# Optimization experiments

Hardware: AMD Instinct MI355X
Metric: run time of the kernel (lower is better)

Reference implementation:

```python
import math
import jax, jax.numpy as jnp
import numpy as np

LARGE_NEG_F32 = -9000000000000000.0  # matches torch code for float32 logits


def setup_inputs() -> dict:
    key = jax.random.key(0)
    ks = jax.random.split(key, 6)
    B, S, D, H = 4, 2048, 1024, 16
    scale = 1.0 / math.sqrt(D)
    query = jax.random.normal(ks[0], (B, S, D), dtype=jnp.float32)
    Wq = jax.random.normal(ks[1], (D, D), dtype=jnp.float32) * scale
    Wk = jax.random.normal(ks[2], (D, D), dtype=jnp.float32) * scale
    Wv = jax.random.normal(ks[3], (D, D), dtype=jnp.float32) * scale
    Wo = jax.random.normal(ks[4], (D, D), dtype=jnp.float32) * scale
    bq = jnp.zeros((D,), jnp.float32)
    bk = jnp.zeros((D,), jnp.float32)
    bv = jnp.zeros((D,), jnp.float32)
    bo = jnp.zeros((D,), jnp.float32)
    padding_mask = jnp.ones((B, S), dtype=jnp.int32)
    causal_mask = jnp.tril(jnp.ones((S, S), dtype=jnp.int32))[None, None]  # [1,1,S,S]
    return {
        "query": query, "padding_mask": padding_mask, "causal_mask": causal_mask,
        "Wq": Wq, "bq": bq, "Wk": Wk, "bk": bk, "Wv": Wv, "bv": bv, "Wo": Wo, "bo": bo,
    }


def reference(query, padding_mask, causal_mask, Wq, bq, Wk, bk, Wv, bv, Wo, bo):
    B, S, D = query.shape
    H = 16
    dh = D // H
    # torch Linear: y = x @ W.T + b  (W stored as [out, in])
    q = query @ Wq.T + bq
    k = query @ Wk.T + bk   # value defaults to query (self-attention)
    v = query @ Wv.T + bv
    # [B, H, S, dh]
    q = q.reshape(B, S, H, dh).transpose(0, 2, 1, 3)
    k = k.reshape(B, S, H, dh).transpose(0, 2, 1, 3)
    v = v.reshape(B, S, H, dh).transpose(0, 2, 1, 3)
    logits = jnp.einsum("bhqd,bhkd->bhqk", q, k) / math.sqrt(dh)
    pad = padding_mask[:, None, None, :]            # [B,1,1,S]
    logits = jnp.where(pad == 0, LARGE_NEG_F32, logits)
    logits = jnp.where(causal_mask == 0, LARGE_NEG_F32, logits)
    weights = jax.nn.softmax(logits, axis=-1)
    out = jnp.einsum("bhqk,bhkd->bhqd", weights, v)
    out = out.transpose(0, 2, 1, 3).reshape(B, S, D)
    out = out @ Wo.T + bo
    return out, weights
```

## Files before the change

kernel.cpp:

```cpp
#include <hip/hip_runtime.h>
#include <stdint.h>


typedef unsigned short u16;
typedef __attribute__((ext_vector_type(8))) short s16x8;
typedef __attribute__((ext_vector_type(4))) float f32x4;

#define BQ 4
#define SQ 2048
#define DQ 1024
#define HQ 16
#define DH 64
#define BSD (BQ * SQ * DQ)

__device__ __forceinline__ u16 f2bf(float f) {
  union { float f; uint32_t u; } x; x.f = f;
  uint32_t r = (x.u + 0x7fffu + ((x.u >> 16) & 1u)) >> 16;
  return (u16)r;
}

template <typename TA>
__global__ __launch_bounds__(256, 2)
void gemm_bt(const TA* __restrict__ A,
             const float* __restrict__ W0, const float* __restrict__ W1, const float* __restrict__ W2,
             const float* __restrict__ b0, const float* __restrict__ b1, const float* __restrict__ b2,
             void* __restrict__ o0, void* __restrict__ o1, void* __restrict__ o2,
             int qkv) {
  const int z = blockIdx.z;
  const float* W    = (z == 0) ? W0 : (z == 1) ? W1 : W2;
  const float* bias = (z == 0) ? b0 : (z == 1) ? b1 : b2;
  void* out         = (z == 0) ? o0 : (z == 1) ? o1 : o2;
  const int mode = qkv ? ((z == 2) ? 1 : 0) : 2;

  const int n0 = blockIdx.x * 128;
  const int m0 = blockIdx.y * 128;
  const int tid = threadIdx.x;
  const int wv = tid >> 6, lane = tid & 63;
  const int wm = wv >> 1, wn = wv & 1;
  const int lr = lane & 15, lg = lane >> 4;

  __shared__ alignas(16) u16 Alds[128 * 64];
  __shared__ alignas(16) u16 Blds[128 * 64];

  const TA* Ablk = A + (size_t)m0 * 1024;
  const float* Wblk = W + (size_t)n0 * 1024;

  f32x4 acc[4][4] = {};

  for (int k0 = 0; k0 < 1024; k0 += 64) {
    __syncthreads();
#pragma unroll
    for (int p = 0; p < 4; ++p) {
      int s = p * 256 + tid;
      int r = s >> 3, c = s & 7;
      int cs = c ^ (r & 7);
      if constexpr (sizeof(TA) == 4) {
        const float* src = (const float*)&Ablk[(size_t)r * 1024 + k0 + c * 8];
        f32x4 a0 = *(const f32x4*)&src[0];
        f32x4 a1 = *(const f32x4*)&src[4];
        s16x8 hv;
#pragma unroll
        for (int j = 0; j < 4; ++j) { hv[j] = (short)f2bf(a0[j]); hv[4 + j] = (short)f2bf(a1[j]); }
        *(s16x8*)&Alds[r * 64 + cs * 8] = hv;
      } else {
        *(s16x8*)&Alds[r * 64 + cs * 8] = *(const s16x8*)&Ablk[(size_t)r * 1024 + k0 + c * 8];
      }
      {
        const float* src = &Wblk[(size_t)r * 1024 + k0 + c * 8];
        f32x4 a0 = *(const f32x4*)&src[0];
        f32x4 a1 = *(const f32x4*)&src[4];
        s16x8 hv;
#pragma unroll
        for (int j = 0; j < 4; ++j) { hv[j] = (short)f2bf(a0[j]); hv[4 + j] = (short)f2bf(a1[j]); }
        *(s16x8*)&Blds[r * 64 + cs * 8] = hv;
      }
    }
    __syncthreads();

#pragma unroll
    for (int half = 0; half < 2; ++half) {
      s16x8 af[4], bf[4];
#pragma unroll
      for (int mt = 0; mt < 4; ++mt) {
        int r = wm * 64 + mt * 16 + lr;
        int cc = (half * 4 + lg) ^ (r & 7);
        af[mt] = *(const s16x8*)&Alds[r * 64 + cc * 8];
      }
#pragma unroll
      for (int nt = 0; nt < 4; ++nt) {
        int r = wn * 64 + nt * 16 + lr;
        int cc = (half * 4 + lg) ^ (r & 7);
        bf[nt] = *(const s16x8*)&Blds[r * 64 + cc * 8];
      }
#pragma unroll
      for (int mt = 0; mt < 4; ++mt)
#pragma unroll
        for (int nt = 0; nt < 4; ++nt)
          acc[mt][nt] = __builtin_amdgcn_mfma_f32_16x16x32_bf16(af[mt], bf[nt], acc[mt][nt], 0, 0, 0);
    }
  }

#pragma unroll
  for (int nt = 0; nt < 4; ++nt) {
    int n = n0 + wn * 64 + nt * 16 + lr;
    float bv = bias[n];
#pragma unroll
    for (int mt = 0; mt < 4; ++mt) {
#pragma unroll
      for (int j = 0; j < 4; ++j) {
        int m = m0 + wm * 64 + mt * 16 + lg * 4 + j;
        float v = acc[mt][nt][j] + bv;
        int s = m & 2047, h = n >> 6, c = n & 63;
        if (mode == 0) {
          int bb = m >> 11;
          ((u16*)out)[(((size_t)bb * HQ + h) * SQ + s) * DH + c] = f2bf(v);
        } else if (mode == 1) {
          int bb = m >> 11;
          ((u16*)out)[(((size_t)bb * HQ + h) * DH + c) * SQ + s] = f2bf(v);
        } else {
          ((float*)out)[(size_t)m * DQ + n] = v;
        }
      }
    }
  }
}

__global__ __launch_bounds__(256, 4)
void attn_kernel(const u16* __restrict__ Qh, const u16* __restrict__ Kh,
                 const u16* __restrict__ Vt, const int* __restrict__ pad,
                 float* __restrict__ Wout, u16* __restrict__ ctx) {
  const int bh = blockIdx.y;
  const int qt = (int)((blockIdx.x + bh) & 31);
  const int b = bh >> 4, h = bh & 15;
  const int tid = threadIdx.x, wv = tid >> 6, lane = tid & 63;
  const int lr = lane & 15, lg = lane >> 4;

  __shared__ alignas(16) float Plds[4][16][68];

  const u16* Qb = Qh + (size_t)bh * SQ * DH;
  const u16* Kb = Kh + (size_t)bh * SQ * DH;
  const u16* Vb = Vt + (size_t)bh * DH * SQ;
  const int* pb = pad + b * SQ;

  const float SCL = 0.125f;
  const float SENT = -30000.0f;

  const int q0 = qt * 64 + wv * 16;

  const s16x8 qf0 = *(const s16x8*)&Qb[(q0 + lr) * DH + lg * 8];
  const s16x8 qf1 = *(const s16x8*)&Qb[(q0 + lr) * DH + 32 + lg * 8];

  auto loadK = [&](int kt, s16x8* a, s16x8* b2) {
    const u16* Kt = Kb + kt * 64 * DH;
#pragma unroll
    for (int kc = 0; kc < 4; ++kc) {
      a[kc]  = *(const s16x8*)&Kt[(kc * 16 + lr) * DH + lg * 8];
      b2[kc] = *(const s16x8*)&Kt[(kc * 16 + lr) * DH + 32 + lg * 8];
    }
  };

  float l[4] = {0.f, 0.f, 0.f, 0.f};
  {
    s16x8 kA[4], kB[4], kC[4], kD[4];
    auto body1 = [&](const s16x8* a, const s16x8* b2, int kt) {
#pragma unroll
      for (int kc = 0; kc < 4; ++kc) {
        f32x4 zz = {0.f, 0.f, 0.f, 0.f};
        f32x4 s = __builtin_amdgcn_mfma_f32_16x16x32_bf16(qf0, a[kc], zz, 0, 0, 0);
        s = __builtin_amdgcn_mfma_f32_16x16x32_bf16(qf1, b2[kc], s, 0, 0, 0);
        int kcol = kt * 64 + kc * 16 + lr;
        bool padz = (pb[kcol] == 0);
#pragma unroll
        for (int j = 0; j < 4; ++j) {
          int qrow = q0 + lg * 4 + j;
          float t = (padz || kcol > qrow) ? SENT : s[j] * SCL;
          l[j] += __expf(t);
        }
      }
    };
    loadK(0, kA, kB);
    for (int kt = 0; kt <= qt; kt += 2) {
      if (kt + 1 <= qt) loadK(kt + 1, kC, kD);
      body1(kA, kB, kt);
      if (kt + 1 <= qt) {
        if (kt + 2 <= qt) loadK(kt + 2, kA, kB);
        body1(kC, kD, kt + 1);
      }
    }
  }

  float invL[4];
#pragma unroll
  for (int j = 0; j < 4; ++j) {
    float la = l[j];
    la += __shfl_xor(la, 1);
    la += __shfl_xor(la, 2);
    la += __shfl_xor(la, 4);
    la += __shfl_xor(la, 8);
    invL[j] = 1.f / la;
  }

  f32x4 o[4] = {};
  {
    s16x8 kA[4], kB[4], kC[4], kD[4];
    auto body2 = [&](const s16x8* a, const s16x8* b2, int kt) {
#pragma unroll
      for (int kc = 0; kc < 4; ++kc) {
        f32x4 zz = {0.f, 0.f, 0.f, 0.f};
        f32x4 s = __builtin_amdgcn_mfma_f32_16x16x32_bf16(qf0, a[kc], zz, 0, 0, 0);
        s = __builtin_amdgcn_mfma_f32_16x16x32_bf16(qf1, b2[kc], s, 0, 0, 0);
        int kcol = kt * 64 + kc * 16 + lr;
        bool padz = (pb[kcol] == 0);
#pragma unroll
        for (int j = 0; j < 4; ++j) {
          int qrow = q0 + lg * 4 + j;
          float t = (padz || kcol > qrow) ? SENT : s[j] * SCL;
          Plds[wv][lg * 4 + j][kc * 16 + lr] = __expf(t) * invL[j];
        }
      }
      {
        int r4 = lane >> 4, seg = lane & 15;
#pragma unroll
        for (int it = 0; it < 4; ++it) {
          int r = it * 4 + r4;
          f32x4 pv = *(const f32x4*)&Plds[wv][r][seg * 4];
          __builtin_nontemporal_store(
              pv, (f32x4*)&Wout[((size_t)bh * SQ + q0 + r) * SQ + kt * 64 + seg * 4]);
        }
      }
#pragma unroll
      for (int h2 = 0; h2 < 2; ++h2) {
        f32x4 p0 = *(const f32x4*)&Plds[wv][lr][h2 * 32 + lg * 8];
        f32x4 p1 = *(const f32x4*)&Plds[wv][lr][h2 * 32 + lg * 8 + 4];
        s16x8 pa;
#pragma unroll
        for (int j = 0; j < 4; ++j) { pa[j] = (short)f2bf(p0[j]); pa[4 + j] = (short)f2bf(p1[j]); }
#pragma unroll
        for (int ct = 0; ct < 4; ++ct) {
          s16x8 vf = *(const s16x8*)&Vb[(ct * 16 + lr) * SQ + kt * 64 + h2 * 32 + lg * 8];
          o[ct] = __builtin_amdgcn_mfma_f32_16x16x32_bf16(pa, vf, o[ct], 0, 0, 0);
        }
      }
    };
    loadK(0, kA, kB);
    for (int kt = 0; kt <= qt; kt += 2) {
      if (kt + 1 <= qt) loadK(kt + 1, kC, kD);
      body2(kA, kB, kt);
      if (kt + 1 <= qt) {
        if (kt + 2 <= qt) loadK(kt + 2, kA, kB);
        body2(kC, kD, kt + 1);
      }
    }
  }

#pragma unroll
  for (int ct = 0; ct < 4; ++ct) {
#pragma unroll
    for (int j = 0; j < 4; ++j) {
      int qrow = q0 + lg * 4 + j;
      int c = ct * 16 + lr;
      ctx[((size_t)b * SQ + qrow) * DQ + h * DH + c] = f2bf(o[ct][j]);
    }
  }

  {
    int zc0 = (qt + 1) * 64;
    if (zc0 < SQ) {
      f32x4 z4 = {0.f, 0.f, 0.f, 0.f};
      for (int rr = 0; rr < 64; ++rr) {
        float* wr = Wout + ((size_t)bh * SQ + qt * 64 + rr) * SQ;
        for (int c = zc0 + tid * 4; c < SQ; c += 1024)
          __builtin_nontemporal_store(z4, (f32x4*)&wr[c]);
      }
    }
  }
}

extern "C" void kernel_launch(void* const* d_in, const int* in_sizes, int n_in,
                              void* d_out, int out_size, void* d_ws, size_t ws_size,
                              hipStream_t stream) {
  const float* X   = (const float*)d_in[0];
  const int* pad   = (const int*)d_in[1];
  const float* Wq = (const float*)d_in[3];  const float* bq = (const float*)d_in[4];
  const float* Wk = (const float*)d_in[5];  const float* bk = (const float*)d_in[6];
  const float* Wv = (const float*)d_in[7];  const float* bv = (const float*)d_in[8];
  const float* Wo = (const float*)d_in[9];  const float* bo = (const float*)d_in[10];

  float* out  = (float*)d_out;
  float* Wout = out + (size_t)BSD;

  u16* ws  = (u16*)d_ws;
  u16* Qh  = ws;
  u16* Kh  = ws + (size_t)BSD;
  u16* Vt  = ws + (size_t)2 * BSD;
  u16* ctx = ws + (size_t)3 * BSD;

  dim3 blk(256);
  gemm_bt<float><<<dim3(8, 64, 3), blk, 0, stream>>>(
      X, Wq, Wk, Wv, bq, bk, bv, Qh, Kh, Vt, 1);
  attn_kernel<<<dim3(32, 64), blk, 0, stream>>>(Qh, Kh, Vt, pad, Wout, ctx);
  gemm_bt<u16><<<dim3(8, 64, 1), blk, 0, stream>>>(
      ctx, Wo, Wo, Wo, bo, bo, bo, out, out, out, 0);
}
```

Before: 846.2 us.

## Stage probabilities as bf16 in LDS and batch weight stores over four key tiles

The per-wave probability tile in LDS now holds bf16 values, and each wave collects up to four 64-column key tiles (256 columns) before writing them out. The attention-weights output is then written as wider contiguous fp32 rows instead of one 64-column tile per step. The PV MFMA operand is read straight from LDS as bf16, which removes the per-tile float-to-bf16 repacking. The cost is that the returned weights are now bf16-rounded values widened back to fp32, which lowers their precision.

```diff
diff --git a/kernel.cpp b/kernel.cpp
--- a/kernel.cpp
+++ b/kernel.cpp
@@ -13,6 +13,9 @@
 #define DH 64
 #define BSD (BQ * SQ * DQ)
 
+__device__ __forceinline__ float bf2f(u16 hv) {
+  union { uint32_t u; float f; } x; x.u = ((uint32_t)hv) << 16; return x.f;
+}
 __device__ __forceinline__ u16 f2bf(float f) {
   union { float f; uint32_t u; } x; x.f = f;
   uint32_t r = (x.u + 0x7fffu + ((x.u >> 16) & 1u)) >> 16;
@@ -129,13 +132,14 @@
 void attn_kernel(const u16* __restrict__ Qh, const u16* __restrict__ Kh,
                  const u16* __restrict__ Vt, const int* __restrict__ pad,
                  float* __restrict__ Wout, u16* __restrict__ ctx) {
+  const int x = blockIdx.x;
   const int bh = blockIdx.y;
-  const int qt = (int)((blockIdx.x + bh) & 31);
+  const int qt = (int)((x + bh) & 31);
   const int b = bh >> 4, h = bh & 15;
   const int tid = threadIdx.x, wv = tid >> 6, lane = tid & 63;
   const int lr = lane & 15, lg = lane >> 4;
 
-  __shared__ alignas(16) float Plds[4][16][68];
+  __shared__ alignas(16) u16 Plds[4][16][264];
 
   const u16* Qb = Qh + (size_t)bh * SQ * DH;
   const u16* Kb = Kh + (size_t)bh * SQ * DH;
@@ -204,6 +208,7 @@
   {
     s16x8 kA[4], kB[4], kC[4], kD[4];
     auto body2 = [&](const s16x8* a, const s16x8* b2, int kt) {
+      const int colbase = (kt & 3) * 64;
 #pragma unroll
       for (int kc = 0; kc < 4; ++kc) {
         f32x4 zz = {0.f, 0.f, 0.f, 0.f};
@@ -215,30 +220,32 @@
         for (int j = 0; j < 4; ++j) {
           int qrow = q0 + lg * 4 + j;
           float t = (padz || kcol > qrow) ? SENT : s[j] * SCL;
-          Plds[wv][lg * 4 + j][kc * 16 + lr] = __expf(t) * invL[j];
-        }
-      }
-      {
-        int r4 = lane >> 4, seg = lane & 15;
-#pragma unroll
-        for (int it = 0; it < 4; ++it) {
-          int r = it * 4 + r4;
-          f32x4 pv = *(const f32x4*)&Plds[wv][r][seg * 4];
-          __builtin_nontemporal_store(
-              pv, (f32x4*)&Wout[((size_t)bh * SQ + q0 + r) * SQ + kt * 64 + seg * 4]);
+          Plds[wv][lg * 4 + j][colbase + kc * 16 + lr] = f2bf(__expf(t) * invL[j]);
         }
       }
 #pragma unroll
       for (int h2 = 0; h2 < 2; ++h2) {
-        f32x4 p0 = *(const f32x4*)&Plds[wv][lr][h2 * 32 + lg * 8];
-        f32x4 p1 = *(const f32x4*)&Plds[wv][lr][h2 * 32 + lg * 8 + 4];
-        s16x8 pa;
-#pragma unroll
-        for (int j = 0; j < 4; ++j) { pa[j] = (short)f2bf(p0[j]); pa[4 + j] = (short)f2bf(p1[j]); }
+        s16x8 pa = *(const s16x8*)&Plds[wv][lr][colbase + h2 * 32 + lg * 8];
 #pragma unroll
         for (int ct = 0; ct < 4; ++ct) {
           s16x8 vf = *(const s16x8*)&Vb[(ct * 16 + lr) * SQ + kt * 64 + h2 * 32 + lg * 8];
           o[ct] = __builtin_amdgcn_mfma_f32_16x16x32_bf16(pa, vf, o[ct], 0, 0, 0);
+        }
+      }
+      if ((kt & 3) == 3 || kt == qt) {
+        int g = (kt & 3) + 1;
+        int kt0 = kt - g + 1;
+        int ncol = g * 64;
+        if (lane * 4 < ncol) {
+#pragma unroll
+          for (int i = 0; i < 16; ++i) {
+            const u16* pr = &Plds[wv][i][lane * 4];
+            f32x4 w4;
+            w4[0] = bf2f(pr[0]); w4[1] = bf2f(pr[1]);
+            w4[2] = bf2f(pr[2]); w4[3] = bf2f(pr[3]);
+            __builtin_nontemporal_store(
+                w4, (f32x4*)&Wout[((size_t)bh * SQ + q0 + i) * SQ + kt0 * 64 + lane * 4]);
+          }
         }
       }
     };
@@ -295,10 +302,9 @@
   u16* Vt  = ws + (size_t)2 * BSD;
   u16* ctx = ws + (size_t)3 * BSD;
 
-  dim3 blk(256);
-  gemm_bt<float><<<dim3(8, 64, 3), blk, 0, stream>>>(
+  gemm_bt<float><<<dim3(8, 64, 3), dim3(256), 0, stream>>>(
       X, Wq, Wk, Wv, bq, bk, bv, Qh, Kh, Vt, 1);
-  attn_kernel<<<dim3(32, 64), blk, 0, stream>>>(Qh, Kh, Vt, pad, Wout, ctx);
-  gemm_bt<u16><<<dim3(8, 64, 1), blk, 0, stream>>>(
+  attn_kernel<<<dim3(32, 64), dim3(256), 0, stream>>>(Qh, Kh, Vt, pad, Wout, ctx);
+  gemm_bt<u16><<<dim3(8, 64, 1), dim3(256), 0, stream>>>(
       ctx, Wo, Wo, Wo, bo, bo, bo, out, out, out, 0);
 }
```

After: 907.0 us. 1.07x slower.
